# Kernel tuning notes

Hardware: AMD Instinct MI355X
Metric: run time of the kernel (lower is better)

The kernel has to match this reference:

```python
import jax, jax.numpy as jnp
import numpy as np

N = 50000      # nodes
E = 800000     # edges (avg degree 16)
DIN = 128
DOUT = 128
L = 8          # num GCN2Conv layers
ALPHA = 0.1
THETA = 0.5


def setup_inputs() -> dict:
    key = jax.random.key(0)
    ks = jax.random.split(key, 5)
    x = jax.random.normal(ks[0], (N, DIN), jnp.float32)
    edge_index = jax.random.randint(ks[1], (2, E), 0, N, dtype=jnp.int64)
    # pre-normalized adjacency weights (normalize=False in GCN2Conv -> adj_t already normalized)
    edge_weight = jax.random.uniform(ks[2], (E,), jnp.float32) / 16.0
    W_lin = jax.random.normal(ks[3], (DIN, DOUT), jnp.float32) / np.sqrt(DIN).astype(np.float32)
    b_lin = jnp.zeros((DOUT,), jnp.float32)
    W_convs = jax.random.normal(ks[4], (L, DOUT, DOUT), jnp.float32) / np.sqrt(DOUT).astype(np.float32)
    return {"x": x, "edge_weight": edge_weight, "W_lin": W_lin, "b_lin": b_lin,
            "W_convs": W_convs, "edge_index": edge_index}


def reference(x, edge_weight, W_lin, b_lin, W_convs, edge_index):
    src, dst = edge_index[0], edge_index[1]
    # betas for GCN2Conv layer l (1-indexed): beta_l = log(theta/l + 1)
    betas = np.log(THETA / np.arange(1, L + 1) + 1.0).astype(np.float32)
    # x = lins(x).relu(); dropout p=0 is a no-op
    x0 = jax.nn.relu(x @ W_lin + b_lin)          # [N, DOUT]
    h = x0
    for l in range(L):
        # sparse propagate: agg = A @ h  (SpMM via gather + segment_sum)
        agg = jax.ops.segment_sum(h[src] * edge_weight[:, None], dst, num_segments=N)
        # initial-residual mixing
        m = (1.0 - ALPHA) * agg + ALPHA * x0
        # identity mapping (shared_weights): out = (1-beta)*m + beta*(m @ W)
        h = jax.nn.relu((1.0 - betas[l]) * m + betas[l] * (m @ W_convs[l]))
    return h
```

## Files before the change

kernel.cpp:

```cpp
#include <hip/hip_runtime.h>
#include <math.h>

#define N_NODES 50000
#define N_EDGES 800000
#define DIM 128
#define PAD 128

typedef __attribute__((ext_vector_type(8))) short short8;
typedef __attribute__((ext_vector_type(4))) float floatx4;

__device__ __forceinline__ unsigned short f32_to_bf16(float f) {
    unsigned int u = __float_as_uint(f);
    u += 0x7fffu + ((u >> 16) & 1u);
    return (unsigned short)(u >> 16);
}
__device__ __forceinline__ float bf16_to_f32(unsigned short h) {
    return __uint_as_float((unsigned int)h << 16);
}


__global__ __launch_bounds__(256) void scatter_pad(const int* __restrict__ src,
                                                   const int* __restrict__ dst,
                                                   const float* __restrict__ ew,
                                                   int* __restrict__ cnt,
                                                   int2* __restrict__ bucket) {
    int e = blockIdx.x * 256 + threadIdx.x;
    if (e < N_EDGES) {
        int d = dst[e];
        int pos = atomicAdd(&cnt[d], 1);
        if (pos < PAD) {
            int2 p; p.x = src[e]; p.y = __float_as_int(ew[e]);
            bucket[(size_t)d * PAD + pos] = p;
        }
    }
}


__global__ __launch_bounds__(256) void spmm8(const unsigned short* __restrict__ hB,
                                             const unsigned short* __restrict__ x0B,
                                             const int* __restrict__ cnt,
                                             const int2* __restrict__ bucket,
                                             unsigned short* __restrict__ mB) {
    int node = blockIdx.x * 4 + (threadIdx.x >> 6);
    int lane = threadIdx.x & 63;
    int eg = lane >> 4;
    int fb = (lane & 15) * 8;
    int end = min(cnt[node], PAD);
    const int2* ep = bucket + (size_t)node * PAD;
    float acc[8] = {0.f, 0.f, 0.f, 0.f, 0.f, 0.f, 0.f, 0.f};
    if (end > 0) {
        int last = end - 1;
        for (int i = 0; i < end; i += 16) {
            int i0 = i + eg, i1 = i0 + 4, i2 = i0 + 8, i3 = i0 + 12;
            int2 e0 = ep[min(i0, last)];
            int2 e1 = ep[min(i1, last)];
            int2 e2 = ep[min(i2, last)];
            int2 e3 = ep[min(i3, last)];
            short8 r0 = *(const short8*)(const void*)(hB + (size_t)e0.x * DIM + fb);
            short8 r1 = *(const short8*)(const void*)(hB + (size_t)e1.x * DIM + fb);
            short8 r2 = *(const short8*)(const void*)(hB + (size_t)e2.x * DIM + fb);
            short8 r3 = *(const short8*)(const void*)(hB + (size_t)e3.x * DIM + fb);
            float w0 = (i0 < end) ? __int_as_float(e0.y) : 0.f;
            float w1 = (i1 < end) ? __int_as_float(e1.y) : 0.f;
            float w2 = (i2 < end) ? __int_as_float(e2.y) : 0.f;
            float w3 = (i3 < end) ? __int_as_float(e3.y) : 0.f;
#pragma unroll
            for (int j = 0; j < 8; j++) {
                acc[j] = fmaf(w0, bf16_to_f32((unsigned short)r0[j]), acc[j]);
                acc[j] = fmaf(w1, bf16_to_f32((unsigned short)r1[j]), acc[j]);
                acc[j] = fmaf(w2, bf16_to_f32((unsigned short)r2[j]), acc[j]);
                acc[j] = fmaf(w3, bf16_to_f32((unsigned short)r3[j]), acc[j]);
            }
        }
    }
#pragma unroll
    for (int j = 0; j < 8; j++) {
        acc[j] += __shfl_down(acc[j], 32);
        acc[j] += __shfl_down(acc[j], 16);
    }
    if (lane < 16) {
        size_t off = (size_t)node * DIM + fb;
        short8 xv = *(const short8*)(const void*)(x0B + off);
        short8 o;
#pragma unroll
        for (int j = 0; j < 8; j++)
            o[j] = (short)f32_to_bf16(0.9f * acc[j]
                                      + 0.1f * bf16_to_f32((unsigned short)xv[j]));
        *(short8*)(void*)(mB + off) = o;
    }
}


template <bool AF32>
__global__ __launch_bounds__(256) void gemm128(const void* __restrict__ Av,
                                               const float* __restrict__ W,
                                               const float* __restrict__ bias,
                                               float* __restrict__ outF,
                                               unsigned short* __restrict__ outB,
                                               float cm, float cg) {
    __shared__ unsigned short WT[128][136];
    for (int idx = threadIdx.x; idx < 128 * 128; idx += 256) {
        int k = idx >> 7, n = idx & 127;
        float wv = cg * W[idx] + ((n == k) ? cm : 0.f);
        WT[n][k] = f32_to_bf16(wv);
    }
    __syncthreads();

    int wave = threadIdx.x >> 6;
    int lane = threadIdx.x & 63;
    int r0 = (blockIdx.x * 4 + wave) * 16;
    if (r0 >= N_NODES) return;

    int mrow = lane & 15;
    int quad = lane >> 4;

    floatx4 acc[8];
#pragma unroll
    for (int t = 0; t < 8; t++) acc[t] = {0.f, 0.f, 0.f, 0.f};

#pragma unroll
    for (int k0 = 0; k0 < 128; k0 += 32) {
        short8 a;
        if constexpr (AF32) {
            const float* arow = (const float*)Av + (size_t)(r0 + mrow) * DIM;
            floatx4 alo = *(const floatx4*)(const void*)(arow + k0 + quad * 8);
            floatx4 ahi = *(const floatx4*)(const void*)(arow + k0 + quad * 8 + 4);
#pragma unroll
            for (int j = 0; j < 4; j++) a[j] = (short)f32_to_bf16(alo[j]);
#pragma unroll
            for (int j = 0; j < 4; j++) a[4 + j] = (short)f32_to_bf16(ahi[j]);
        } else {
            const unsigned short* arow = (const unsigned short*)Av + (size_t)(r0 + mrow) * DIM;
            a = *(const short8*)(const void*)(arow + k0 + quad * 8);
        }
#pragma unroll
        for (int t = 0; t < 8; t++) {
            short8 b = *(const short8*)(const void*)(&WT[t * 16 + mrow][k0 + quad * 8]);
            acc[t] = __builtin_amdgcn_mfma_f32_16x16x32_bf16(a, b, acc[t], 0, 0, 0);
        }
    }

#pragma unroll
    for (int t = 0; t < 8; t++) {
        int col = t * 16 + mrow;
        float bv = bias ? bias[col] : 0.f;
#pragma unroll
        for (int i = 0; i < 4; i++) {
            int row = r0 + quad * 4 + i;
            size_t off = (size_t)row * DIM + col;
            float v = fmaxf(acc[t][i] + bv, 0.f);
            if (outF) outF[off] = v;
            if (outB) outB[off] = f32_to_bf16(v);
        }
    }
}


extern "C" void kernel_launch(void* const* d_in, const int* in_sizes, int n_in,
                              void* d_out, int out_size, void* d_ws, size_t ws_size,
                              hipStream_t stream) {
    const float* x    = (const float*)d_in[0];
    const float* ew   = (const float*)d_in[1];
    const float* Wlin = (const float*)d_in[2];
    const float* blin = (const float*)d_in[3];
    const float* Wcv  = (const float*)d_in[4];
    const int* eidx = (const int*)d_in[5];
    const int* esrc = eidx;
    const int* edst = eidx + N_EDGES;
    float* out = (float*)d_out;

    char* ws = (char*)d_ws;
    unsigned short* x0B = (unsigned short*)(ws);
    unsigned short* mB  = (unsigned short*)(ws + 12800000);
    unsigned short* hB  = (unsigned short*)(ws + 25600000);
    int* cnt            = (int*)(ws + 38400000);
    int2* bucket        = (int2*)(ws + 38600064);

    const int grid = (N_NODES + 63) / 64;

    gemm128<true><<<grid, 256, 0, stream>>>(x, Wlin, blin, nullptr, x0B, 0.f, 1.f);

    (void)hipMemsetAsync(cnt, 0, N_NODES * sizeof(int), stream);
    scatter_pad<<<(N_EDGES + 255) / 256, 256, 0, stream>>>(esrc, edst, ew, cnt, bucket);

    const unsigned short* hin = x0B;
    for (int l = 0; l < 8; l++) {
        spmm8<<<N_NODES / 4, 256, 0, stream>>>(hin, x0B, cnt, bucket, mB);
        float beta = logf(0.5f / (float)(l + 1) + 1.f);
        gemm128<false><<<grid, 256, 0, stream>>>(mB, Wcv + (size_t)l * DIM * DIM, nullptr,
                                                 (l == 7) ? out : nullptr,
                                                 (l < 7) ? hB : nullptr,
                                                 1.f - beta, beta);
        hin = hB;
    }
}
```

Measured before the change: 499.7 us.

## Fuse SpMM with per-layer GEMM and precompute bf16 weight transposes

Merges each layer's sparse aggregation and dense 128x128 transform into one kernel: 32 aggregated rows are staged in shared memory and multiplied immediately, so the intermediate m matrix never makes a round trip through global memory. Weight transposes, beta folding and the counter reset move into a single prep kernel. The edge scatter and the first linear layer share one launch, which removes a memset and several kernel launches. In exchange, bucket padding drops to 120, which could silently drop edges at high-degree nodes, and h is ping-ponged between two buffers.

```diff
diff --git a/kernel.cpp b/kernel.cpp
--- a/kernel.cpp
+++ b/kernel.cpp
@@ -4,7 +4,9 @@
 #define N_NODES 50000
 #define N_EDGES 800000
 #define DIM 128
-#define PAD 128
+#define PAD 120
+#define SCATTER_BLOCKS 3125
+#define GEMM0_BLOCKS 782
 
 typedef __attribute__((ext_vector_type(8))) short short8;
 typedef __attribute__((ext_vector_type(4))) float floatx4;
@@ -18,139 +20,198 @@
     return __uint_as_float((unsigned int)h << 16);
 }
 
-
-__global__ __launch_bounds__(256) void scatter_pad(const int* __restrict__ src,
-                                                   const int* __restrict__ dst,
-                                                   const float* __restrict__ ew,
-                                                   int* __restrict__ cnt,
-                                                   int2* __restrict__ bucket) {
-    int e = blockIdx.x * 256 + threadIdx.x;
-    if (e < N_EDGES) {
-        int d = dst[e];
-        int pos = atomicAdd(&cnt[d], 1);
-        if (pos < PAD) {
-            int2 p; p.x = src[e]; p.y = __float_as_int(ew[e]);
-            bucket[(size_t)d * PAD + pos] = p;
-        }
-    }
-}
-
-
-__global__ __launch_bounds__(256) void spmm8(const unsigned short* __restrict__ hB,
-                                             const unsigned short* __restrict__ x0B,
-                                             const int* __restrict__ cnt,
-                                             const int2* __restrict__ bucket,
-                                             unsigned short* __restrict__ mB) {
-    int node = blockIdx.x * 4 + (threadIdx.x >> 6);
-    int lane = threadIdx.x & 63;
-    int eg = lane >> 4;
-    int fb = (lane & 15) * 8;
-    int end = min(cnt[node], PAD);
-    const int2* ep = bucket + (size_t)node * PAD;
-    float acc[8] = {0.f, 0.f, 0.f, 0.f, 0.f, 0.f, 0.f, 0.f};
-    if (end > 0) {
-        int last = end - 1;
-        for (int i = 0; i < end; i += 16) {
-            int i0 = i + eg, i1 = i0 + 4, i2 = i0 + 8, i3 = i0 + 12;
-            int2 e0 = ep[min(i0, last)];
-            int2 e1 = ep[min(i1, last)];
-            int2 e2 = ep[min(i2, last)];
-            int2 e3 = ep[min(i3, last)];
-            short8 r0 = *(const short8*)(const void*)(hB + (size_t)e0.x * DIM + fb);
-            short8 r1 = *(const short8*)(const void*)(hB + (size_t)e1.x * DIM + fb);
-            short8 r2 = *(const short8*)(const void*)(hB + (size_t)e2.x * DIM + fb);
-            short8 r3 = *(const short8*)(const void*)(hB + (size_t)e3.x * DIM + fb);
-            float w0 = (i0 < end) ? __int_as_float(e0.y) : 0.f;
-            float w1 = (i1 < end) ? __int_as_float(e1.y) : 0.f;
-            float w2 = (i2 < end) ? __int_as_float(e2.y) : 0.f;
-            float w3 = (i3 < end) ? __int_as_float(e3.y) : 0.f;
-#pragma unroll
-            for (int j = 0; j < 8; j++) {
-                acc[j] = fmaf(w0, bf16_to_f32((unsigned short)r0[j]), acc[j]);
-                acc[j] = fmaf(w1, bf16_to_f32((unsigned short)r1[j]), acc[j]);
-                acc[j] = fmaf(w2, bf16_to_f32((unsigned short)r2[j]), acc[j]);
-                acc[j] = fmaf(w3, bf16_to_f32((unsigned short)r3[j]), acc[j]);
-            }
-        }
-    }
-#pragma unroll
-    for (int j = 0; j < 8; j++) {
-        acc[j] += __shfl_down(acc[j], 32);
-        acc[j] += __shfl_down(acc[j], 16);
-    }
-    if (lane < 16) {
-        size_t off = (size_t)node * DIM + fb;
-        short8 xv = *(const short8*)(const void*)(x0B + off);
-        short8 o;
-#pragma unroll
-        for (int j = 0; j < 8; j++)
-            o[j] = (short)f32_to_bf16(0.9f * acc[j]
-                                      + 0.1f * bf16_to_f32((unsigned short)xv[j]));
-        *(short8*)(void*)(mB + off) = o;
-    }
-}
-
-
-template <bool AF32>
-__global__ __launch_bounds__(256) void gemm128(const void* __restrict__ Av,
-                                               const float* __restrict__ W,
-                                               const float* __restrict__ bias,
-                                               float* __restrict__ outF,
-                                               unsigned short* __restrict__ outB,
-                                               float cm, float cg) {
+__global__ __launch_bounds__(256) void prep(const float* __restrict__ Wlin,
+                                            const float* __restrict__ Wcv,
+                                            int* __restrict__ cnt,
+                                            unsigned short* __restrict__ WTg) {
+    int i = blockIdx.x * 256 + threadIdx.x;
+    if (i < N_NODES) cnt[i] = 0;
+    int m = i >> 14;
+    int n = (i >> 7) & 127;
+    int k = i & 127;
+    float v;
+    if (m == 0) {
+        v = Wlin[k * 128 + n];
+    } else {
+        int l = m - 1;
+        float beta = logf(0.5f / (float)(l + 1) + 1.0f);
+        v = beta * Wcv[(size_t)l * 16384 + k * 128 + n]
+            + ((n == k) ? (1.0f - beta) : 0.0f);
+    }
+    WTg[i] = f32_to_bf16(v);
+}
+
+__global__ __launch_bounds__(256) void fat0(const float* __restrict__ x,
+                                            const unsigned short* __restrict__ WTg,
+                                            const float* __restrict__ bias,
+                                            unsigned short* __restrict__ x0B,
+                                            const int* __restrict__ src,
+                                            const int* __restrict__ dst,
+                                            const float* __restrict__ ew,
+                                            int* __restrict__ cnt,
+                                            int2* __restrict__ bucket) {
+    if (blockIdx.x < SCATTER_BLOCKS) {
+        int e = blockIdx.x * 256 + threadIdx.x;
+        if (e < N_EDGES) {
+            int d = dst[e];
+            int pos = atomicAdd(&cnt[d], 1);
+            if (pos < PAD) {
+                int2 p; p.x = src[e]; p.y = __float_as_int(ew[e]);
+                bucket[(size_t)d * PAD + pos] = p;
+            }
+        }
+        return;
+    }
     __shared__ unsigned short WT[128][136];
-    for (int idx = threadIdx.x; idx < 128 * 128; idx += 256) {
-        int k = idx >> 7, n = idx & 127;
-        float wv = cg * W[idx] + ((n == k) ? cm : 0.f);
-        WT[n][k] = f32_to_bf16(wv);
+    for (int idx = threadIdx.x; idx < 2048; idx += 256) {
+        int n = idx >> 4, c = idx & 15;
+        *(short8*)(void*)&WT[n][c * 8] =
+            *(const short8*)(const void*)(WTg + n * 128 + c * 8);
     }
     __syncthreads();
-
     int wave = threadIdx.x >> 6;
     int lane = threadIdx.x & 63;
-    int r0 = (blockIdx.x * 4 + wave) * 16;
+    int r0 = ((blockIdx.x - SCATTER_BLOCKS) * 4 + wave) * 16;
     if (r0 >= N_NODES) return;
-
     int mrow = lane & 15;
     int quad = lane >> 4;
-
     floatx4 acc[8];
 #pragma unroll
     for (int t = 0; t < 8; t++) acc[t] = {0.f, 0.f, 0.f, 0.f};
-
 #pragma unroll
     for (int k0 = 0; k0 < 128; k0 += 32) {
+        const float* arow = x + (size_t)(r0 + mrow) * DIM;
+        floatx4 alo = *(const floatx4*)(const void*)(arow + k0 + quad * 8);
+        floatx4 ahi = *(const floatx4*)(const void*)(arow + k0 + quad * 8 + 4);
         short8 a;
-        if constexpr (AF32) {
-            const float* arow = (const float*)Av + (size_t)(r0 + mrow) * DIM;
-            floatx4 alo = *(const floatx4*)(const void*)(arow + k0 + quad * 8);
-            floatx4 ahi = *(const floatx4*)(const void*)(arow + k0 + quad * 8 + 4);
-#pragma unroll
-            for (int j = 0; j < 4; j++) a[j] = (short)f32_to_bf16(alo[j]);
-#pragma unroll
-            for (int j = 0; j < 4; j++) a[4 + j] = (short)f32_to_bf16(ahi[j]);
-        } else {
-            const unsigned short* arow = (const unsigned short*)Av + (size_t)(r0 + mrow) * DIM;
-            a = *(const short8*)(const void*)(arow + k0 + quad * 8);
-        }
+#pragma unroll
+        for (int j = 0; j < 4; j++) a[j] = (short)f32_to_bf16(alo[j]);
+#pragma unroll
+        for (int j = 0; j < 4; j++) a[4 + j] = (short)f32_to_bf16(ahi[j]);
 #pragma unroll
         for (int t = 0; t < 8; t++) {
             short8 b = *(const short8*)(const void*)(&WT[t * 16 + mrow][k0 + quad * 8]);
             acc[t] = __builtin_amdgcn_mfma_f32_16x16x32_bf16(a, b, acc[t], 0, 0, 0);
         }
     }
-
 #pragma unroll
     for (int t = 0; t < 8; t++) {
         int col = t * 16 + mrow;
-        float bv = bias ? bias[col] : 0.f;
+        float bv = bias[col];
 #pragma unroll
         for (int i = 0; i < 4; i++) {
             int row = r0 + quad * 4 + i;
-            size_t off = (size_t)row * DIM + col;
             float v = fmaxf(acc[t][i] + bv, 0.f);
-            if (outF) outF[off] = v;
-            if (outB) outB[off] = f32_to_bf16(v);
+            x0B[(size_t)row * DIM + col] = f32_to_bf16(v);
+        }
+    }
+}
+
+__global__ __launch_bounds__(512, 4) void layer_fused(
+        const unsigned short* __restrict__ hB,
+        const unsigned short* __restrict__ x0B,
+        const int* __restrict__ cnt,
+        const int2* __restrict__ bucket,
+        const unsigned short* __restrict__ WTg,
+        float* __restrict__ outF,
+        unsigned short* __restrict__ outB) {
+    __shared__ unsigned short WT[128][136];
+    __shared__ unsigned short M[32][136];
+    int tid = threadIdx.x;
+    for (int idx = tid; idx < 2048; idx += 512) {
+        int n = idx >> 4, c = idx & 15;
+        *(short8*)(void*)&WT[n][c * 8] =
+            *(const short8*)(const void*)(WTg + n * 128 + c * 8);
+    }
+    int wave = tid >> 6;
+    int lane = tid & 63;
+    int eg = lane >> 4;
+    int fb = (lane & 15) * 8;
+    int r0 = blockIdx.x * 32;
+
+    for (int s = 0; s < 4; s++) {
+        int row = (wave << 2) + s;
+        int node = r0 + row;
+        float acc[8] = {0.f, 0.f, 0.f, 0.f, 0.f, 0.f, 0.f, 0.f};
+        if (node < N_NODES) {
+            int end = min(cnt[node], PAD);
+            if (end > 0) {
+                const int2* ep = bucket + (size_t)node * PAD;
+                int last = end - 1;
+                for (int i = 0; i < end; i += 16) {
+                    int i0 = i + eg, i1 = i0 + 4, i2 = i0 + 8, i3 = i0 + 12;
+                    int2 e0 = ep[min(i0, last)];
+                    int2 e1 = ep[min(i1, last)];
+                    int2 e2 = ep[min(i2, last)];
+                    int2 e3 = ep[min(i3, last)];
+                    short8 r0v = *(const short8*)(const void*)(hB + (size_t)e0.x * DIM + fb);
+                    short8 r1v = *(const short8*)(const void*)(hB + (size_t)e1.x * DIM + fb);
+                    short8 r2v = *(const short8*)(const void*)(hB + (size_t)e2.x * DIM + fb);
+                    short8 r3v = *(const short8*)(const void*)(hB + (size_t)e3.x * DIM + fb);
+                    float w0 = (i0 < end) ? __int_as_float(e0.y) : 0.f;
+                    float w1 = (i1 < end) ? __int_as_float(e1.y) : 0.f;
+                    float w2 = (i2 < end) ? __int_as_float(e2.y) : 0.f;
+                    float w3 = (i3 < end) ? __int_as_float(e3.y) : 0.f;
+#pragma unroll
+                    for (int j = 0; j < 8; j++) {
+                        acc[j] = fmaf(w0, bf16_to_f32((unsigned short)r0v[j]), acc[j]);
+                        acc[j] = fmaf(w1, bf16_to_f32((unsigned short)r1v[j]), acc[j]);
+                        acc[j] = fmaf(w2, bf16_to_f32((unsigned short)r2v[j]), acc[j]);
+                        acc[j] = fmaf(w3, bf16_to_f32((unsigned short)r3v[j]), acc[j]);
+                    }
+                }
+            }
+        }
+#pragma unroll
+        for (int j = 0; j < 8; j++) {
+            acc[j] += __shfl_down(acc[j], 32);
+            acc[j] += __shfl_down(acc[j], 16);
+        }
+        if (lane < 16) {
+            short8 o;
+            if (node < N_NODES) {
+                short8 xv = *(const short8*)(const void*)(x0B + (size_t)node * DIM + fb);
+#pragma unroll
+                for (int j = 0; j < 8; j++)
+                    o[j] = (short)f32_to_bf16(0.9f * acc[j]
+                                              + 0.1f * bf16_to_f32((unsigned short)xv[j]));
+            } else {
+#pragma unroll
+                for (int j = 0; j < 8; j++) o[j] = 0;
+            }
+            *(short8*)(void*)&M[row][fb] = o;
+        }
+    }
+    __syncthreads();
+
+    int mrow = lane & 15;
+    int quad = lane >> 4;
+    int rt = wave >> 2;
+    int ctb = (wave & 3) * 2;
+    floatx4 acc2[2];
+    acc2[0] = {0.f, 0.f, 0.f, 0.f};
+    acc2[1] = {0.f, 0.f, 0.f, 0.f};
+#pragma unroll
+    for (int k0 = 0; k0 < 128; k0 += 32) {
+        short8 a = *(const short8*)(const void*)(&M[rt * 16 + mrow][k0 + quad * 8]);
+#pragma unroll
+        for (int t = 0; t < 2; t++) {
+            short8 b = *(const short8*)(const void*)(&WT[(ctb + t) * 16 + mrow][k0 + quad * 8]);
+            acc2[t] = __builtin_amdgcn_mfma_f32_16x16x32_bf16(a, b, acc2[t], 0, 0, 0);
+        }
+    }
+#pragma unroll
+    for (int t = 0; t < 2; t++) {
+        int col = (ctb + t) * 16 + mrow;
+#pragma unroll
+        for (int i = 0; i < 4; i++) {
+            int row = r0 + rt * 16 + quad * 4 + i;
+            if (row < N_NODES) {
+                float v = fmaxf(acc2[t][i], 0.f);
+                size_t off = (size_t)row * DIM + col;
+                if (outF) outF[off] = v;
+                if (outB) outB[off] = f32_to_bf16(v);
+            }
         }
     }
 }
@@ -171,26 +232,23 @@
 
     char* ws = (char*)d_ws;
     unsigned short* x0B = (unsigned short*)(ws);
-    unsigned short* mB  = (unsigned short*)(ws + 12800000);
-    unsigned short* hB  = (unsigned short*)(ws + 25600000);
+    unsigned short* hA  = (unsigned short*)(ws + 12800000);
+    unsigned short* hB2 = (unsigned short*)(ws + 25600000);
     int* cnt            = (int*)(ws + 38400000);
     int2* bucket        = (int2*)(ws + 38600064);
-
-    const int grid = (N_NODES + 63) / 64;
-
-    gemm128<true><<<grid, 256, 0, stream>>>(x, Wlin, blin, nullptr, x0B, 0.f, 1.f);
-
-    (void)hipMemsetAsync(cnt, 0, N_NODES * sizeof(int), stream);
-    scatter_pad<<<(N_EDGES + 255) / 256, 256, 0, stream>>>(esrc, edst, ew, cnt, bucket);
+    unsigned short* WTg = (unsigned short*)(ws + 86600064);
+
+    prep<<<576, 256, 0, stream>>>(Wlin, Wcv, cnt, WTg);
+
+    fat0<<<SCATTER_BLOCKS + GEMM0_BLOCKS, 256, 0, stream>>>(x, WTg, blin, x0B,
+                                                            esrc, edst, ew, cnt, bucket);
 
     const unsigned short* hin = x0B;
     for (int l = 0; l < 8; l++) {
-        spmm8<<<N_NODES / 4, 256, 0, stream>>>(hin, x0B, cnt, bucket, mB);
-        float beta = logf(0.5f / (float)(l + 1) + 1.f);
-        gemm128<false><<<grid, 256, 0, stream>>>(mB, Wcv + (size_t)l * DIM * DIM, nullptr,
-                                                 (l == 7) ? out : nullptr,
-                                                 (l < 7) ? hB : nullptr,
-                                                 1.f - beta, beta);
-        hin = hB;
-    }
-}
+        unsigned short* hout = (l == 7) ? nullptr : ((l & 1) ? hB2 : hA);
+        layer_fused<<<1563, 512, 0, stream>>>(hin, x0B, cnt, bucket,
+                                              WTg + (size_t)(1 + l) * 16384,
+                                              (l == 7) ? out : nullptr, hout);
+        hin = hout;
+    }
+}
```

After: 481.3 us. 1.04x faster.
